# Kernel optimization log

Measured on AMD Instinct MI355X. Metric: run time of the kernel, lower is better.

Reference implementation:

```python
import jax, jax.numpy as jnp
from jax import lax
import numpy as np

ALPHA = 0.5      # convex-combination rate from __init__ default
DECAY = 0.9
B, IN, H, OUT, K = 8192, 512, 512, 256, 3


def setup_inputs() -> dict:
    key = jax.random.key(0)
    ks = jax.random.split(key, 8)
    sc = 1.0 / np.sqrt(IN)
    sh = 1.0 / np.sqrt(H)
    return {
        "x": jax.random.normal(ks[0], (B, IN), jnp.float32),
        "Wx_w": jax.random.normal(ks[1], (H, IN), jnp.float32) * sc,
        "Wx_b": jax.random.normal(ks[2], (H,), jnp.float32) * sc,
        # orthogonal-ish, scaled by 0.9 like nn.init.orthogonal_ + mul_(0.9)
        "Wh_w": 0.9 * jnp.linalg.qr(jax.random.normal(ks[3], (H, H), jnp.float32))[0],
        "Wh_b": jax.random.normal(ks[4], (H,), jnp.float32) * sh,
        "Head_w": jax.random.normal(ks[5], (OUT, H), jnp.float32) * sh,
        "Head_b": jax.random.normal(ks[6], (OUT,), jnp.float32) * sh,
        "buffer_gamma": jnp.asarray(0.1, jnp.float32),
        "alphas": jnp.asarray([DECAY ** (k + 1) for k in range(K)], jnp.float32),
        "steps": 30,
    }


def reference(x, Wx_w, Wx_b, Wh_w, Wh_b, Head_w, Head_b, buffer_gamma, alphas, steps):
    batch = x.shape[0]
    hidden = Wh_w.shape[0]
    k_hist = alphas.shape[0]
    # Wx(x) is constant across steps -> hoist out of the loop (same math)
    xproj = x @ Wx_w.T + Wx_b                      # [B, H]
    stack0 = jnp.zeros((batch, k_hist + 1, hidden), x.dtype)  # [B, K+1, H]

    def step(stack, _):
        s_t = stack[:, 0]                          # [B, H]
        history = stack[:, 1:]                     # [B, K, H]
        recirc = jnp.einsum('bkh,k->bh', history, alphas)
        pre_act = xproj + s_t @ Wh_w.T + Wh_b + buffer_gamma * recirc
        h_new = jnp.tanh(pre_act)
        s_next = (1.0 - ALPHA) * s_t + ALPHA * h_new
        new_stack = jnp.concatenate(
            [s_next[:, None], s_t[:, None], history[:, :-1]], axis=1)
        return new_stack, None

    stack, _ = lax.scan(step, stack0, None, length=steps)
    return stack[:, 0] @ Head_w.T + Head_b         # [B, OUT]
```

## Files before the change

kernel.cpp:

```cpp
#include <hip/hip_runtime.h>
#include <hip/hip_bf16.h>

typedef __attribute__((ext_vector_type(8))) short short8;
typedef __attribute__((ext_vector_type(4))) float f32x4;
typedef unsigned long long u64;

#define THREADS 512
#define MFMA(a, b, c) __builtin_amdgcn_mfma_f32_16x16x32_bf16((a), (b), (c), 0, 0, 0)

static __device__ __forceinline__ unsigned short f2bf(float x) {
    __hip_bfloat16 h = __float2bfloat16(x);
    return __builtin_bit_cast(unsigned short, h);
}
static __device__ __forceinline__ unsigned pk2(float a, float b) {
    return (unsigned)f2bf(a) | ((unsigned)f2bf(b) << 16);
}
static __device__ __forceinline__ float bflo(unsigned u) {
    unsigned v = u << 16; return __builtin_bit_cast(float, v);
}
static __device__ __forceinline__ float bfhi(unsigned u) {
    unsigned v = u & 0xffff0000u; return __builtin_bit_cast(float, v);
}
static __device__ __forceinline__ float fast_tanh(float x) {
    float e = __builtin_amdgcn_exp2f(x * 2.885390081777927f);
    float r = __builtin_amdgcn_rcpf(e + 1.0f);
    return fmaf(-2.0f, r, 1.0f);
}
static __device__ __forceinline__ short8 cvt8(float4 a, float4 b) {
    short8 r;
    r[0] = (short)f2bf(a.x); r[1] = (short)f2bf(a.y);
    r[2] = (short)f2bf(a.z); r[3] = (short)f2bf(a.w);
    r[4] = (short)f2bf(b.x); r[5] = (short)f2bf(b.y);
    r[6] = (short)f2bf(b.z); r[7] = (short)f2bf(b.w);
    return r;
}
static __device__ __forceinline__ u64 ld_sys(const u64* p) {
    return __hip_atomic_load(p, __ATOMIC_RELAXED, __HIP_MEMORY_SCOPE_SYSTEM);
}
static __device__ __forceinline__ void st_sys(u64* p, u64 v) {
    __hip_atomic_store(p, v, __ATOMIC_RELAXED, __HIP_MEMORY_SCOPE_SYSTEM);
}
static __device__ __forceinline__ int ldf(const int* p) {
    return __hip_atomic_load(p, __ATOMIC_RELAXED, __HIP_MEMORY_SCOPE_SYSTEM);
}
static __device__ __forceinline__ void stf(int* p, int v) {
    __hip_atomic_store(p, v, __ATOMIC_RELAXED, __HIP_MEMORY_SCOPE_SYSTEM);
}
#define WAITV0() asm volatile("s_waitcnt vmcnt(0)" ::: "memory")

#define LOAD_PANEL(W, CB, KT_OF_J)                                              \
    do {                                                                        \
        _Pragma("unroll")                                                       \
        for (int j = 0; j < 16; ++j) {                                          \
            const int kt_ = (KT_OF_J);                                          \
            const float* p0_ = (W) + (size_t)((CB) + c) * 512 + kt_ * 32 + q * 8;       \
            const float* p1_ = (W) + (size_t)((CB) + 16 + c) * 512 + kt_ * 32 + q * 8;  \
            float4 a0_ = *(const float4*)p0_, b0_ = *(const float4*)(p0_ + 4);  \
            float4 a1_ = *(const float4*)p1_, b1_ = *(const float4*)(p1_ + 4);  \
            bw0[j] = cvt8(a0_, b0_);                                            \
            bw1[j] = cvt8(a1_, b1_);                                            \
        }                                                                       \
    } while (0)

template<bool DBUF>
__global__ __attribute__((amdgpu_flat_work_group_size(512, 512), amdgpu_waves_per_eu(2, 2)))
void toroidal(
    const float* __restrict__ x,
    const float* __restrict__ Wx_w, const float* __restrict__ wxb,
    const float* __restrict__ Wh_w, const float* __restrict__ whb,
    const float* __restrict__ Hd_w, const float* __restrict__ hdb,
    const float* __restrict__ gamma_p, const float* __restrict__ alphas,
    const int* __restrict__ steps_p,
    float* __restrict__ out, int* __restrict__ flags,
    unsigned short* __restrict__ pieces, size_t slotStride )
{
    __shared__ __align__(16) unsigned short sfrag[32768];
    __shared__ __align__(16) unsigned int   hist[16384];

    const int tid = threadIdx.x;
    const int w = tid >> 6;
    const int l = tid & 63;
    const int q = l >> 4;
    const int c = l & 15;

    const int bi  = blockIdx.x;
    const int mu  = (bi >> 3) & 1;
    const int grp = (bi & 7) * 16 + (bi >> 4);
    const int pb  = bi ^ 8;
    const int rows0 = grp * 64;

    int* prod = flags;
    int* cons = flags + 256;

    unsigned short* pbase = pieces + (size_t)grp * 32768 + mu * 16384;
    const unsigned short* qbase = pieces + (size_t)grp * 32768 + (1 - mu) * 16384;

    const float gm = gamma_p[0];
    const float g1 = gm * alphas[0], g2 = gm * alphas[1], g3 = gm * alphas[2];
    const int nsteps = steps_p[0];

    const int colbase = mu * 256 + w * 32;
    const float bias0 = wxb[colbase + c] + whb[colbase + c];
    const float bias1 = wxb[colbase + 16 + c] + whb[colbase + 16 + c];
    const float hb0 = hdb[w * 32 + c], hb1 = hdb[w * 32 + 16 + c];

    const int roff = l * 8;
    const int k0own = 8 * mu, k0par = 8 * (1 - mu);

    short8 bw0[16], bw1[16];

    LOAD_PANEL(Wx_w, colbase, j);

    f32x4 acc[4][2];
    #pragma unroll
    for (int mt = 0; mt < 4; ++mt) {
        acc[mt][0] = (f32x4){0.f, 0.f, 0.f, 0.f};
        acc[mt][1] = (f32x4){0.f, 0.f, 0.f, 0.f};
    }
    #pragma unroll
    for (int pass = 0; pass < 2; ++pass) {
        __syncthreads();
        #pragma unroll
        for (int j2 = 0; j2 < 8; ++j2) {
            int r = j2 * 8 + w;
            int kloc = l * 4;
            float4 v = *(const float4*)(x + (size_t)(rows0 + r) * 512 + pass * 256 + kloc);
            int mtx = r >> 4, ktl = kloc >> 5;
            int lane2 = (r & 15) + 16 * ((kloc >> 3) & 3);
            float* dst = (float*)sfrag + ((mtx * 8 + ktl) * 64 + lane2) * 8 + (kloc & 7);
            *(float4*)dst = v;
        }
        __syncthreads();
        #pragma unroll
        for (int j = 0; j < 8; ++j) {
            #pragma unroll
            for (int mt = 0; mt < 4; ++mt) {
                const float* fp = (const float*)sfrag + ((mt * 8 + j) * 64 + l) * 8;
                float4 u0 = *(const float4*)fp;
                float4 u1 = *(const float4*)(fp + 4);
                short8 a = cvt8(u0, u1);
                acc[mt][0] = MFMA(a, bw0[pass * 8 + j], acc[mt][0]);
                acc[mt][1] = MFMA(a, bw1[pass * 8 + j], acc[mt][1]);
            }
        }
    }
    __syncthreads();

    unsigned xpk[4][2][2];
    #pragma unroll
    for (int mt = 0; mt < 4; ++mt)
        #pragma unroll
        for (int nt = 0; nt < 2; ++nt) {
            float b = nt ? bias1 : bias0;
            xpk[mt][nt][0] = pk2(acc[mt][nt][0] + b, acc[mt][nt][1] + b);
            xpk[mt][nt][1] = pk2(acc[mt][nt][2] + b, acc[mt][nt][3] + b);
        }

    LOAD_PANEL(Wh_w, colbase, (j < 8 ? k0own + j : k0par + (j - 8)));

    uint4 z4 = {0u, 0u, 0u, 0u};
    #pragma unroll
    for (int sb = 0; sb < 8; ++sb) *(uint4*)&hist[(sb * 512 + tid) * 4] = z4;
    float s[4][2][4];
    unsigned h0[4][2][2];
    #pragma unroll
    for (int mt = 0; mt < 4; ++mt)
        #pragma unroll
        for (int nt = 0; nt < 2; ++nt) {
            acc[mt][nt] = (f32x4){0.f, 0.f, 0.f, 0.f};
            h0[mt][nt][0] = h0[mt][nt][1] = 0u;
            #pragma unroll
            for (int i = 0; i < 4; ++i) s[mt][nt][i] = 0.f;
        }

    for (int t = 1; t <= nsteps; ++t) {
        const int sA = t & 1, sB = sA ^ 1;
        #pragma unroll
        for (int mt = 0; mt < 4; ++mt) {
            uint4 hA = *(uint4*)&hist[((sA * 4 + mt) * 512 + tid) * 4];
            uint4 hB = *(uint4*)&hist[((sB * 4 + mt) * 512 + tid) * 4];
            uint4 nB;
            #pragma unroll
            for (int nt = 0; nt < 2; ++nt)
                #pragma unroll
                for (int pi = 0; pi < 2; ++pi) {
                    unsigned u1 = h0[mt][nt][pi];
                    unsigned u2 = ((unsigned*)&hA)[nt * 2 + pi];
                    unsigned u3 = ((unsigned*)&hB)[nt * 2 + pi];
                    unsigned ux = xpk[mt][nt][pi];
                    float p0 = acc[mt][nt][pi * 2] + bflo(ux)
                             + g1 * bflo(u1) + g2 * bflo(u2) + g3 * bflo(u3);
                    float p1 = acc[mt][nt][pi * 2 + 1] + bfhi(ux)
                             + g1 * bfhi(u1) + g2 * bfhi(u2) + g3 * bfhi(u3);
                    float so0 = s[mt][nt][pi * 2], so1 = s[mt][nt][pi * 2 + 1];
                    float sn0 = 0.5f * so0 + 0.5f * fast_tanh(p0);
                    float sn1 = 0.5f * so1 + 0.5f * fast_tanh(p1);
                    s[mt][nt][pi * 2] = sn0; s[mt][nt][pi * 2 + 1] = sn1;
                    ((unsigned*)&nB)[nt * 2 + pi] = u1;
                    h0[mt][nt][pi] = pk2(so0, so1);
                }
            *(uint4*)&hist[((sB * 4 + mt) * 512 + tid) * 4] = nB;
            acc[mt][0] = (f32x4){0.f, 0.f, 0.f, 0.f};
            acc[mt][1] = (f32x4){0.f, 0.f, 0.f, 0.f};
        }

        #pragma unroll
        for (int mt = 0; mt < 4; ++mt)
            #pragma unroll
            for (int nt = 0; nt < 2; ++nt)
                #pragma unroll
                for (int i = 0; i < 4; ++i) {
                    int lam = q * 4 + i + 16 * (nt * 2 + (c >> 3));
                    sfrag[(mt * 16 + k0own + w) * 512 + lam * 8 + (c & 7)] = f2bf(s[mt][nt][i]);
                }
        __syncthreads();

        if (!DBUF) {
            if (l == 0) { while (ldf(&cons[pb]) < t - 1) __builtin_amdgcn_s_sleep(2); }
            __builtin_amdgcn_sched_barrier(0);
        }

        u64* dstp = (u64*)(pbase + (DBUF ? (size_t)(t & 1) * slotStride : 0));
        #pragma unroll
        for (int i = 0; i < 8; ++i) {
            int u = i * 512 + tid;
            int mtg = u >> 10, ktl = (u >> 7) & 7, off = (u & 127) * 4;
            u64 v = *(const u64*)&sfrag[(mtg * 16 + k0own + ktl) * 512 + off];
            st_sys(dstp + u, v);
        }

        if (t == nsteps) {
            WAITV0();
            __builtin_amdgcn_s_barrier();
            if (tid == 0) stf(&prod[bi], t);
            break;
        }

        #pragma unroll
        for (int j = 0; j < 8; ++j) {
            const int kt = k0own + j;
            short8 a0 = *(const short8*)&sfrag[(0 * 16 + kt) * 512 + roff];
            short8 a1 = *(const short8*)&sfrag[(1 * 16 + kt) * 512 + roff];
            short8 a2 = *(const short8*)&sfrag[(2 * 16 + kt) * 512 + roff];
            short8 a3 = *(const short8*)&sfrag[(3 * 16 + kt) * 512 + roff];
            acc[0][0] = MFMA(a0, bw0[j], acc[0][0]); acc[0][1] = MFMA(a0, bw1[j], acc[0][1]);
            acc[1][0] = MFMA(a1, bw0[j], acc[1][0]); acc[1][1] = MFMA(a1, bw1[j], acc[1][1]);
            acc[2][0] = MFMA(a2, bw0[j], acc[2][0]); acc[2][1] = MFMA(a2, bw1[j], acc[2][1]);
            acc[3][0] = MFMA(a3, bw0[j], acc[3][0]); acc[3][1] = MFMA(a3, bw1[j], acc[3][1]);
        }

        WAITV0();
        __builtin_amdgcn_s_barrier();
        if (tid == 0) stf(&prod[bi], t);

        if (l == 0) { while (ldf(&prod[pb]) < t) __builtin_amdgcn_s_sleep(2); }
        __builtin_amdgcn_sched_barrier(0);
        {
            const u64* srcp = (const u64*)(qbase + (DBUF ? (size_t)(t & 1) * slotStride : 0));
            u64 tmp[8];
            #pragma unroll
            for (int i = 0; i < 8; ++i) tmp[i] = ld_sys(srcp + i * 512 + tid);
            #pragma unroll
            for (int i = 0; i < 8; ++i) {
                int u = i * 512 + tid;
                int mtg = u >> 10, ktl = (u >> 7) & 7, off = (u & 127) * 4;
                *(u64*)&sfrag[(mtg * 16 + k0par + ktl) * 512 + off] = tmp[i];
            }
        }
        __syncthreads();
        if (!DBUF) { if (tid == 0) stf(&cons[bi], t); }

        #pragma unroll
        for (int j = 8; j < 16; ++j) {
            const int kt = k0par + (j - 8);
            short8 a0 = *(const short8*)&sfrag[(0 * 16 + kt) * 512 + roff];
            short8 a1 = *(const short8*)&sfrag[(1 * 16 + kt) * 512 + roff];
            short8 a2 = *(const short8*)&sfrag[(2 * 16 + kt) * 512 + roff];
            short8 a3 = *(const short8*)&sfrag[(3 * 16 + kt) * 512 + roff];
            acc[0][0] = MFMA(a0, bw0[j], acc[0][0]); acc[0][1] = MFMA(a0, bw1[j], acc[0][1]);
            acc[1][0] = MFMA(a1, bw0[j], acc[1][0]); acc[1][1] = MFMA(a1, bw1[j], acc[1][1]);
            acc[2][0] = MFMA(a2, bw0[j], acc[2][0]); acc[2][1] = MFMA(a2, bw1[j], acc[2][1]);
            acc[3][0] = MFMA(a3, bw0[j], acc[3][0]); acc[3][1] = MFMA(a3, bw1[j], acc[3][1]);
        }
    }

    if (l == 0) { while (ldf(&prod[pb]) < nsteps) __builtin_amdgcn_s_sleep(2); }
    __builtin_amdgcn_sched_barrier(0);
    {
        const u64* srcp = (const u64*)(qbase + (DBUF ? (size_t)(nsteps & 1) * slotStride : 0));
        u64 tmp[8];
        #pragma unroll
        for (int i = 0; i < 8; ++i) tmp[i] = ld_sys(srcp + i * 512 + tid);
        #pragma unroll
        for (int i = 0; i < 8; ++i) {
            int u = i * 512 + tid;
            int mtg = u >> 10, ktl = (u >> 7) & 7, off = (u & 127) * 4;
            *(u64*)&sfrag[(mtg * 16 + k0par + ktl) * 512 + off] = tmp[i];
        }
    }
    LOAD_PANEL(Hd_w, w * 32, (j < 8 ? k0own + j : k0par + (j - 8)));
    __syncthreads();
    if (!DBUF) { if (tid == 0) stf(&cons[bi], nsteps); }

    f32x4 ah[2][2];
    ah[0][0] = (f32x4){0.f, 0.f, 0.f, 0.f}; ah[0][1] = (f32x4){0.f, 0.f, 0.f, 0.f};
    ah[1][0] = (f32x4){0.f, 0.f, 0.f, 0.f}; ah[1][1] = (f32x4){0.f, 0.f, 0.f, 0.f};
    #pragma unroll
    for (int j = 0; j < 16; ++j) {
        const int kt = (j < 8) ? k0own + j : k0par + (j - 8);
        short8 a0 = *(const short8*)&sfrag[((2 * mu + 0) * 16 + kt) * 512 + roff];
        short8 a1 = *(const short8*)&sfrag[((2 * mu + 1) * 16 + kt) * 512 + roff];
        ah[0][0] = MFMA(a0, bw0[j], ah[0][0]); ah[0][1] = MFMA(a0, bw1[j], ah[0][1]);
        ah[1][0] = MFMA(a1, bw0[j], ah[1][0]); ah[1][1] = MFMA(a1, bw1[j], ah[1][1]);
    }

    if (!DBUF) {
        if (l == 0) { while (ldf(&cons[pb]) < nsteps) __builtin_amdgcn_s_sleep(2); }
        __builtin_amdgcn_sched_barrier(0);
    }
    #pragma unroll
    for (int mtL = 0; mtL < 2; ++mtL)
        #pragma unroll
        for (int i = 0; i < 4; ++i) {
            int r = rows0 + 32 * mu + mtL * 16 + q * 4 + i;
            out[(size_t)r * 256 + w * 32 + c]      = ah[mtL][0][i] + hb0;
            out[(size_t)r * 256 + w * 32 + 16 + c] = ah[mtL][1][i] + hb1;
        }
}

extern "C" void kernel_launch(void* const* d_in, const int* in_sizes, int n_in,
                              void* d_out, int out_size, void* d_ws, size_t ws_size,
                              hipStream_t stream) {
    (void)n_in; (void)out_size;
    const float* x    = (const float*)d_in[0];
    const float* Wx_w = (const float*)d_in[1];
    const float* Wx_b = (const float*)d_in[2];
    const float* Wh_w = (const float*)d_in[3];
    const float* Wh_b = (const float*)d_in[4];
    const float* Hd_w = (const float*)d_in[5];
    const float* Hd_b = (const float*)d_in[6];
    const float* gma  = (const float*)d_in[7];
    const float* alp  = (const float*)d_in[8];
    const int*   stp  = (const int*)d_in[9];
    float* out = (float*)d_out;

    if (ws_size < 4096) return;
    int* flags = (int*)d_ws;
    hipMemsetAsync(flags, 0, 4096, stream);

    const size_t SLOT = (size_t)8 << 20;
    int batch = in_sizes[0] / 512;
    int nblk  = batch / 32;

    if (ws_size >= 4096 + 2 * SLOT) {
        unsigned short* pieces = (unsigned short*)((char*)d_ws + 4096);
        toroidal<true><<<nblk, THREADS, 0, stream>>>(x, Wx_w, Wx_b, Wh_w, Wh_b, Hd_w, Hd_b,
                                                     gma, alp, stp, out, flags,
                                                     pieces, SLOT / 2);
    } else if (ws_size >= 4096 + SLOT) {
        unsigned short* pieces = (unsigned short*)((char*)d_ws + 4096);
        toroidal<false><<<nblk, THREADS, 0, stream>>>(x, Wx_w, Wx_b, Wh_w, Wh_b, Hd_w, Hd_b,
                                                      gma, alp, stp, out, flags,
                                                      pieces, 0);
    } else {
        toroidal<false><<<nblk, THREADS, 0, stream>>>(x, Wx_w, Wx_b, Wh_w, Wh_b, Hd_w, Hd_b,
                                                      gma, alp, stp, out, flags,
                                                      (unsigned short*)out, 0);
    }
}
```

Baseline: 574.1 us.

## Use per-wave fine-grained flags and split-half exchange to overlap partner communication

Replaces block-wide producer/consumer flags with per-wave flags, so each wave publishes its slice of the new state as soon as that half of the elementwise update is done. The partner block then waits only on the specific wave flags it needs. The partner-half GEMM is split in two so the second-half global loads overlap the first-half MFMAs. This aims to cut barrier and flag-polling latency on the critical path of each recurrent step, at the cost of more flag traffic and more complex ordering that could race if any flag is misplaced.

```diff
diff --git a/kernel.cpp b/kernel.cpp
--- a/kernel.cpp
+++ b/kernel.cpp
@@ -46,7 +46,12 @@
 static __device__ __forceinline__ void stf(int* p, int v) {
     __hip_atomic_store(p, v, __ATOMIC_RELAXED, __HIP_MEMORY_SCOPE_SYSTEM);
 }
-#define WAITV0() asm volatile("s_waitcnt vmcnt(0)" ::: "memory")
+static __device__ __forceinline__ u64 pku(unsigned lo, unsigned hi) {
+    return (u64)lo | ((u64)hi << 32);
+}
+#define WAITV0()  asm volatile("s_waitcnt vmcnt(0)" ::: "memory")
+#define WAITLG0() asm volatile("s_waitcnt lgkmcnt(0)" ::: "memory")
+#define SCHEDB()  __builtin_amdgcn_sched_barrier(0)
 
 #define LOAD_PANEL(W, CB, KT_OF_J)                                              \
     do {                                                                        \
@@ -62,6 +67,79 @@
         }                                                                       \
     } while (0)
 
+#define EW_HALF(h)                                                              \
+    do {                                                                        \
+        _Pragma("unroll")                                                       \
+        for (int mt = 2*(h); mt < 2*(h) + 2; ++mt) {                            \
+            uint4 hA = *(uint4*)&hist[((sA * 4 + mt) * 512 + tid) * 4];         \
+            uint4 hB = *(uint4*)&hist[((sB * 4 + mt) * 512 + tid) * 4];         \
+            uint4 nB;                                                           \
+            _Pragma("unroll")                                                   \
+            for (int nt = 0; nt < 2; ++nt)                                      \
+                _Pragma("unroll")                                               \
+                for (int pi = 0; pi < 2; ++pi) {                                \
+                    unsigned u1 = h0[mt][nt][pi];                               \
+                    unsigned u2 = ((unsigned*)&hA)[nt * 2 + pi];                \
+                    unsigned u3 = ((unsigned*)&hB)[nt * 2 + pi];                \
+                    unsigned ux = xpk[mt][nt][pi];                              \
+                    float p0 = acc[mt][nt][pi * 2] + bflo(ux)                   \
+                             + g1 * bflo(u1) + g2 * bflo(u2) + g3 * bflo(u3);   \
+                    float p1 = acc[mt][nt][pi * 2 + 1] + bfhi(ux)               \
+                             + g1 * bfhi(u1) + g2 * bfhi(u2) + g3 * bfhi(u3);   \
+                    float so0 = s[mt][nt][pi * 2], so1 = s[mt][nt][pi * 2 + 1]; \
+                    float sn0 = 0.5f * so0 + 0.5f * fast_tanh(p0);              \
+                    float sn1 = 0.5f * so1 + 0.5f * fast_tanh(p1);              \
+                    s[mt][nt][pi * 2] = sn0; s[mt][nt][pi * 2 + 1] = sn1;       \
+                    ((unsigned*)&nB)[nt * 2 + pi] = u1;                         \
+                    h0[mt][nt][pi] = pk2(so0, so1);                             \
+                }                                                               \
+            *(uint4*)&hist[((sB * 4 + mt) * 512 + tid) * 4] = nB;               \
+            acc[mt][0] = (f32x4){0.f, 0.f, 0.f, 0.f};                           \
+            acc[mt][1] = (f32x4){0.f, 0.f, 0.f, 0.f};                           \
+        }                                                                       \
+    } while (0)
+
+#define SCATTER_HALF(h)                                                         \
+    do {                                                                        \
+        _Pragma("unroll")                                                       \
+        for (int mt = 2*(h); mt < 2*(h) + 2; ++mt)                              \
+            _Pragma("unroll")                                                   \
+            for (int nt = 0; nt < 2; ++nt)                                      \
+                _Pragma("unroll")                                               \
+                for (int i = 0; i < 4; ++i) {                                   \
+                    int lam = q * 4 + i + 16 * (nt * 2 + (c >> 3));             \
+                    sfrag[(mt * 16 + k0own + w) * 512 + lam * 8 + (c & 7)] =    \
+                        f2bf(s[mt][nt][i]);                                     \
+                }                                                               \
+    } while (0)
+
+#define CP_POST(h, tt, myslot)                                                  \
+    do {                                                                        \
+        WAITLG0(); SCHEDB();                                                    \
+        uint4 vA = *(const uint4*)&sfrag[((2*(h)) * 16 + k0own + w) * 512 + l * 8];     \
+        uint4 vB = *(const uint4*)&sfrag[((2*(h)+1) * 16 + k0own + w) * 512 + l * 8];   \
+        u64* dA = (u64*)((myslot) + ((2*(h)) * 8 + w) * 512 + l * 8);           \
+        u64* dB = (u64*)((myslot) + ((2*(h)+1) * 8 + w) * 512 + l * 8);         \
+        st_sys(dA, pku(vA.x, vA.y)); st_sys(dA + 1, pku(vA.z, vA.w));           \
+        st_sys(dB, pku(vB.x, vB.y)); st_sys(dB + 1, pku(vB.z, vB.w));           \
+        WAITV0();                                                               \
+        if (l == 0) stf(&prodw[bi * 8 + w], 2 * (tt) + (h));                    \
+    } while (0)
+
+#define PGEMM_HALF(h)                                                           \
+    do {                                                                        \
+        _Pragma("unroll")                                                       \
+        for (int j = 0; j < 8; ++j) {                                           \
+            const int kt = k0par + j;                                           \
+            short8 aL = *(const short8*)&sfrag[((2*(h)) * 16 + kt) * 512 + roff];       \
+            short8 aH = *(const short8*)&sfrag[((2*(h)+1) * 16 + kt) * 512 + roff];     \
+            acc[2*(h)][0]   = MFMA(aL, bw0[8 + j], acc[2*(h)][0]);              \
+            acc[2*(h)][1]   = MFMA(aL, bw1[8 + j], acc[2*(h)][1]);              \
+            acc[2*(h)+1][0] = MFMA(aH, bw0[8 + j], acc[2*(h)+1][0]);            \
+            acc[2*(h)+1][1] = MFMA(aH, bw1[8 + j], acc[2*(h)+1][1]);            \
+        }                                                                       \
+    } while (0)
+
 template<bool DBUF>
 __global__ __attribute__((amdgpu_flat_work_group_size(512, 512), amdgpu_waves_per_eu(2, 2)))
 void toroidal(
@@ -72,7 +150,7 @@
     const float* __restrict__ gamma_p, const float* __restrict__ alphas,
     const int* __restrict__ steps_p,
     float* __restrict__ out, int* __restrict__ flags,
-    unsigned short* __restrict__ pieces, size_t slotStride )
+    unsigned short* __restrict__ slotE, unsigned short* __restrict__ slotO)
 {
     __shared__ __align__(16) unsigned short sfrag[32768];
     __shared__ __align__(16) unsigned int   hist[16384];
@@ -89,11 +167,14 @@
     const int pb  = bi ^ 8;
     const int rows0 = grp * 64;
 
-    int* prod = flags;
-    int* cons = flags + 256;
-
-    unsigned short* pbase = pieces + (size_t)grp * 32768 + mu * 16384;
-    const unsigned short* qbase = pieces + (size_t)grp * 32768 + (1 - mu) * 16384;
+    int* prodw = flags;
+    int* consw = flags + 2048;
+    int* consB = flags + 4096;
+
+    unsigned short* myE = slotE + (size_t)grp * 32768 + mu * 16384;
+    unsigned short* myO = slotO + (size_t)grp * 32768 + mu * 16384;
+    const unsigned short* qE = slotE + (size_t)grp * 32768 + (1 - mu) * 16384;
+    const unsigned short* qO = slotO + (size_t)grp * 32768 + (1 - mu) * 16384;
 
     const float gm = gamma_p[0];
     const float g1 = gm * alphas[0], g2 = gm * alphas[1], g3 = gm * alphas[2];
@@ -173,68 +254,33 @@
             for (int i = 0; i < 4; ++i) s[mt][nt][i] = 0.f;
         }
 
+    const int cmt_lo = (w >> 2);
+    const int ktl0 = (2 * w) & 7;
+
     for (int t = 1; t <= nsteps; ++t) {
         const int sA = t & 1, sB = sA ^ 1;
-        #pragma unroll
-        for (int mt = 0; mt < 4; ++mt) {
-            uint4 hA = *(uint4*)&hist[((sA * 4 + mt) * 512 + tid) * 4];
-            uint4 hB = *(uint4*)&hist[((sB * 4 + mt) * 512 + tid) * 4];
-            uint4 nB;
-            #pragma unroll
-            for (int nt = 0; nt < 2; ++nt)
-                #pragma unroll
-                for (int pi = 0; pi < 2; ++pi) {
-                    unsigned u1 = h0[mt][nt][pi];
-                    unsigned u2 = ((unsigned*)&hA)[nt * 2 + pi];
-                    unsigned u3 = ((unsigned*)&hB)[nt * 2 + pi];
-                    unsigned ux = xpk[mt][nt][pi];
-                    float p0 = acc[mt][nt][pi * 2] + bflo(ux)
-                             + g1 * bflo(u1) + g2 * bflo(u2) + g3 * bflo(u3);
-                    float p1 = acc[mt][nt][pi * 2 + 1] + bfhi(ux)
-                             + g1 * bfhi(u1) + g2 * bfhi(u2) + g3 * bfhi(u3);
-                    float so0 = s[mt][nt][pi * 2], so1 = s[mt][nt][pi * 2 + 1];
-                    float sn0 = 0.5f * so0 + 0.5f * fast_tanh(p0);
-                    float sn1 = 0.5f * so1 + 0.5f * fast_tanh(p1);
-                    s[mt][nt][pi * 2] = sn0; s[mt][nt][pi * 2 + 1] = sn1;
-                    ((unsigned*)&nB)[nt * 2 + pi] = u1;
-                    h0[mt][nt][pi] = pk2(so0, so1);
-                }
-            *(uint4*)&hist[((sB * 4 + mt) * 512 + tid) * 4] = nB;
-            acc[mt][0] = (f32x4){0.f, 0.f, 0.f, 0.f};
-            acc[mt][1] = (f32x4){0.f, 0.f, 0.f, 0.f};
-        }
-
-        #pragma unroll
-        for (int mt = 0; mt < 4; ++mt)
-            #pragma unroll
-            for (int nt = 0; nt < 2; ++nt)
-                #pragma unroll
-                for (int i = 0; i < 4; ++i) {
-                    int lam = q * 4 + i + 16 * (nt * 2 + (c >> 3));
-                    sfrag[(mt * 16 + k0own + w) * 512 + lam * 8 + (c & 7)] = f2bf(s[mt][nt][i]);
-                }
+        unsigned short* us = (t & 1) ? myO : myE;
+        const unsigned short* qs = (t & 1) ? qO : qE;
+
+        if (!DBUF && t >= 2) {
+            const int wA = (w & 6) >> 1, wB = wA + 4, tv = 2 * (t - 1) + 1;
+            if (l == 0) {
+                while (ldf(&consw[pb * 8 + wA]) < tv || ldf(&consw[pb * 8 + wB]) < tv)
+                    __builtin_amdgcn_s_sleep(1);
+            }
+            SCHEDB();
+        }
+
+        EW_HALF(0);
+        SCATTER_HALF(0);
+        CP_POST(0, t, us);
+        EW_HALF(1);
+        SCATTER_HALF(1);
+        CP_POST(1, t, us);
+
+        if (t == nsteps) break;
+
         __syncthreads();
-
-        if (!DBUF) {
-            if (l == 0) { while (ldf(&cons[pb]) < t - 1) __builtin_amdgcn_s_sleep(2); }
-            __builtin_amdgcn_sched_barrier(0);
-        }
-
-        u64* dstp = (u64*)(pbase + (DBUF ? (size_t)(t & 1) * slotStride : 0));
-        #pragma unroll
-        for (int i = 0; i < 8; ++i) {
-            int u = i * 512 + tid;
-            int mtg = u >> 10, ktl = (u >> 7) & 7, off = (u & 127) * 4;
-            u64 v = *(const u64*)&sfrag[(mtg * 16 + k0own + ktl) * 512 + off];
-            st_sys(dstp + u, v);
-        }
-
-        if (t == nsteps) {
-            WAITV0();
-            __builtin_amdgcn_s_barrier();
-            if (tid == 0) stf(&prod[bi], t);
-            break;
-        }
 
         #pragma unroll
         for (int j = 0; j < 8; ++j) {
@@ -249,58 +295,89 @@
             acc[3][0] = MFMA(a3, bw0[j], acc[3][0]); acc[3][1] = MFMA(a3, bw1[j], acc[3][1]);
         }
 
-        WAITV0();
-        __builtin_amdgcn_s_barrier();
-        if (tid == 0) stf(&prod[bi], t);
-
-        if (l == 0) { while (ldf(&prod[pb]) < t) __builtin_amdgcn_s_sleep(2); }
-        __builtin_amdgcn_sched_barrier(0);
         {
-            const u64* srcp = (const u64*)(qbase + (DBUF ? (size_t)(t & 1) * slotStride : 0));
-            u64 tmp[8];
-            #pragma unroll
-            for (int i = 0; i < 8; ++i) tmp[i] = ld_sys(srcp + i * 512 + tid);
-            #pragma unroll
-            for (int i = 0; i < 8; ++i) {
-                int u = i * 512 + tid;
-                int mtg = u >> 10, ktl = (u >> 7) & 7, off = (u & 127) * 4;
-                *(u64*)&sfrag[(mtg * 16 + k0par + ktl) * 512 + off] = tmp[i];
+            const int mt = cmt_lo;
+            const int v = 2 * t;
+            if (l == 0) {
+                for (;;) {
+                    u64 f = ld_sys((const u64*)&prodw[pb * 8 + ktl0]);
+                    if ((int)(f & 0xffffffffu) >= v && (int)(f >> 32) >= v) break;
+                    __builtin_amdgcn_s_sleep(1);
+                }
             }
+            SCHEDB();
+            const u64* s0 = (const u64*)(qs + (mt * 8 + ktl0) * 512 + l * 8);
+            const u64* s1 = (const u64*)(qs + (mt * 8 + ktl0 + 1) * 512 + l * 8);
+            u64 a0 = ld_sys(s0), a1 = ld_sys(s0 + 1);
+            u64 b0 = ld_sys(s1), b1 = ld_sys(s1 + 1);
+            uint4 wA = { (unsigned)a0, (unsigned)(a0 >> 32), (unsigned)a1, (unsigned)(a1 >> 32) };
+            uint4 wB = { (unsigned)b0, (unsigned)(b0 >> 32), (unsigned)b1, (unsigned)(b1 >> 32) };
+            *(uint4*)&sfrag[(mt * 16 + k0par + ktl0) * 512 + l * 8]       = wA;
+            *(uint4*)&sfrag[(mt * 16 + k0par + ktl0 + 1) * 512 + l * 8]   = wB;
         }
         __syncthreads();
-        if (!DBUF) { if (tid == 0) stf(&cons[bi], t); }
-
-        #pragma unroll
-        for (int j = 8; j < 16; ++j) {
-            const int kt = k0par + (j - 8);
-            short8 a0 = *(const short8*)&sfrag[(0 * 16 + kt) * 512 + roff];
-            short8 a1 = *(const short8*)&sfrag[(1 * 16 + kt) * 512 + roff];
-            short8 a2 = *(const short8*)&sfrag[(2 * 16 + kt) * 512 + roff];
-            short8 a3 = *(const short8*)&sfrag[(3 * 16 + kt) * 512 + roff];
-            acc[0][0] = MFMA(a0, bw0[j], acc[0][0]); acc[0][1] = MFMA(a0, bw1[j], acc[0][1]);
-            acc[1][0] = MFMA(a1, bw0[j], acc[1][0]); acc[1][1] = MFMA(a1, bw1[j], acc[1][1]);
-            acc[2][0] = MFMA(a2, bw0[j], acc[2][0]); acc[2][1] = MFMA(a2, bw1[j], acc[2][1]);
-            acc[3][0] = MFMA(a3, bw0[j], acc[3][0]); acc[3][1] = MFMA(a3, bw1[j], acc[3][1]);
-        }
-    }
-
-    if (l == 0) { while (ldf(&prod[pb]) < nsteps) __builtin_amdgcn_s_sleep(2); }
-    __builtin_amdgcn_sched_barrier(0);
+
+        u64 c0, c1, d0, d1;
+        {
+            const int mt = 2 + cmt_lo;
+            const int v = 2 * t + 1;
+            if (l == 0) {
+                for (;;) {
+                    u64 f = ld_sys((const u64*)&prodw[pb * 8 + ktl0]);
+                    if ((int)(f & 0xffffffffu) >= v && (int)(f >> 32) >= v) break;
+                    __builtin_amdgcn_s_sleep(1);
+                }
+            }
+            SCHEDB();
+            const u64* s0 = (const u64*)(qs + (mt * 8 + ktl0) * 512 + l * 8);
+            const u64* s1 = (const u64*)(qs + (mt * 8 + ktl0 + 1) * 512 + l * 8);
+            c0 = ld_sys(s0); c1 = ld_sys(s0 + 1);
+            d0 = ld_sys(s1); d1 = ld_sys(s1 + 1);
+        }
+
+        PGEMM_HALF(0);
+
+        {
+            const int mt = 2 + cmt_lo;
+            uint4 wA = { (unsigned)c0, (unsigned)(c0 >> 32), (unsigned)c1, (unsigned)(c1 >> 32) };
+            uint4 wB = { (unsigned)d0, (unsigned)(d0 >> 32), (unsigned)d1, (unsigned)(d1 >> 32) };
+            *(uint4*)&sfrag[(mt * 16 + k0par + ktl0) * 512 + l * 8]     = wA;
+            *(uint4*)&sfrag[(mt * 16 + k0par + ktl0 + 1) * 512 + l * 8] = wB;
+        }
+        __syncthreads();
+
+        PGEMM_HALF(1);
+
+        if (!DBUF) { if (l == 0) stf(&consw[bi * 8 + w], 2 * t + 1); }
+    }
+
     {
-        const u64* srcp = (const u64*)(qbase + (DBUF ? (size_t)(nsteps & 1) * slotStride : 0));
-        u64 tmp[8];
-        #pragma unroll
-        for (int i = 0; i < 8; ++i) tmp[i] = ld_sys(srcp + i * 512 + tid);
-        #pragma unroll
-        for (int i = 0; i < 8; ++i) {
-            int u = i * 512 + tid;
-            int mtg = u >> 10, ktl = (u >> 7) & 7, off = (u & 127) * 4;
-            *(u64*)&sfrag[(mtg * 16 + k0par + ktl) * 512 + off] = tmp[i];
+        const int fb = 4 * (w & 1);
+        const int v = 2 * nsteps + 1;
+        if (l == 0) {
+            for (;;) {
+                u64 f0 = ld_sys((const u64*)&prodw[pb * 8 + fb]);
+                u64 f1 = ld_sys((const u64*)&prodw[pb * 8 + fb + 2]);
+                if ((int)(f0 & 0xffffffffu) >= v && (int)(f0 >> 32) >= v &&
+                    (int)(f1 & 0xffffffffu) >= v && (int)(f1 >> 32) >= v) break;
+                __builtin_amdgcn_s_sleep(1);
+            }
+        }
+        SCHEDB();
+        const unsigned short* qs = (nsteps & 1) ? qO : qE;
+        const int mtg = w >> 1;
+        #pragma unroll
+        for (int i2 = 0; i2 < 4; ++i2) {
+            const int ktl = fb + i2;
+            const u64* sp = (const u64*)(qs + (mtg * 8 + ktl) * 512 + l * 8);
+            u64 a0 = ld_sys(sp), a1 = ld_sys(sp + 1);
+            uint4 vv = { (unsigned)a0, (unsigned)(a0 >> 32), (unsigned)a1, (unsigned)(a1 >> 32) };
+            *(uint4*)&sfrag[(mtg * 16 + k0par + ktl) * 512 + l * 8] = vv;
         }
     }
     LOAD_PANEL(Hd_w, w * 32, (j < 8 ? k0own + j : k0par + (j - 8)));
     __syncthreads();
-    if (!DBUF) { if (tid == 0) stf(&cons[bi], nsteps); }
+    if (!DBUF) { if (tid == 0) stf(&consB[bi], 1); }
 
     f32x4 ah[2][2];
     ah[0][0] = (f32x4){0.f, 0.f, 0.f, 0.f}; ah[0][1] = (f32x4){0.f, 0.f, 0.f, 0.f};
@@ -315,8 +392,8 @@
     }
 
     if (!DBUF) {
-        if (l == 0) { while (ldf(&cons[pb]) < nsteps) __builtin_amdgcn_s_sleep(2); }
-        __builtin_amdgcn_sched_barrier(0);
+        if (l == 0) { while (ldf(&consB[pb]) < 1) __builtin_amdgcn_s_sleep(1); }
+        SCHEDB();
     }
     #pragma unroll
     for (int mtL = 0; mtL < 2; ++mtL)
@@ -344,27 +421,28 @@
     const int*   stp  = (const int*)d_in[9];
     float* out = (float*)d_out;
 
-    if (ws_size < 4096) return;
+    const size_t FB   = 20480;
+    const size_t SLOT = (size_t)8 * 1024 * 1024;
+    if (ws_size < FB) return;
     int* flags = (int*)d_ws;
-    hipMemsetAsync(flags, 0, 4096, stream);
-
-    const size_t SLOT = (size_t)8 << 20;
+    hipMemsetAsync(flags, 0, FB, stream);
+
     int batch = in_sizes[0] / 512;
     int nblk  = batch / 32;
 
-    if (ws_size >= 4096 + 2 * SLOT) {
-        unsigned short* pieces = (unsigned short*)((char*)d_ws + 4096);
+    if (ws_size >= FB + 2 * SLOT) {
+        unsigned short* e = (unsigned short*)((char*)d_ws + FB);
+        unsigned short* o = e + SLOT / 2;
+        toroidal<true><<<nblk, THREADS, 0, stream>>>(x, Wx_w, Wx_b, Wh_w, Wh_b, Hd_w, Hd_b,
+                                                     gma, alp, stp, out, flags, e, o);
+    } else if (ws_size >= FB + SLOT) {
+        unsigned short* e = (unsigned short*)((char*)d_ws + FB);
         toroidal<true><<<nblk, THREADS, 0, stream>>>(x, Wx_w, Wx_b, Wh_w, Wh_b, Hd_w, Hd_b,
                                                      gma, alp, stp, out, flags,
-                                                     pieces, SLOT / 2);
-    } else if (ws_size >= 4096 + SLOT) {
-        unsigned short* pieces = (unsigned short*)((char*)d_ws + 4096);
-        toroidal<false><<<nblk, THREADS, 0, stream>>>(x, Wx_w, Wx_b, Wh_w, Wh_b, Hd_w, Hd_b,
-                                                      gma, alp, stp, out, flags,
-                                                      pieces, 0);
+                                                     e, (unsigned short*)out);
     } else {
         toroidal<false><<<nblk, THREADS, 0, stream>>>(x, Wx_w, Wx_b, Wh_w, Wh_b, Hd_w, Hd_b,
                                                       gma, alp, stp, out, flags,
-                                                      (unsigned short*)out, 0);
-    }
-}
+                                                      (unsigned short*)out, (unsigned short*)out);
+    }
+}
```

Result: faster. 542.8 us (-5.4%).
